# Optimization experiments

Measured on AMD Instinct MI355X. Metric: run time of the kernel, lower is better.

## Reference

```python
import jax, jax.numpy as jnp
import numpy as np

B, L, D, Y = 8, 2500, 512, 8921


def setup_inputs() -> dict:
    key = jax.random.key(0)
    k1, k2, k3, k4, k5, k6 = jax.random.split(key, 6)
    x = jax.random.normal(k1, (B, L, D), dtype=jnp.float32)
    target = jax.random.uniform(k2, (B, Y), dtype=jnp.float32)
    text_inputs = jax.random.randint(k3, (B, L), 0, 50000, dtype=jnp.int32)
    # Xavier-uniform-like init for the two [Y, D] weights
    lim = float(np.sqrt(6.0 / (Y + D)))
    U_weight = jax.random.uniform(k4, (Y, D), dtype=jnp.float32, minval=-lim, maxval=lim)
    final_weight = jax.random.uniform(k5, (Y, D), dtype=jnp.float32, minval=-lim, maxval=lim)
    final_bias = jax.random.uniform(k6, (Y,), dtype=jnp.float32, minval=-0.05, maxval=0.05)
    return {"x": x, "target": target, "text_inputs": text_inputs,
            "U_weight": U_weight, "final_weight": final_weight, "final_bias": final_bias}


def reference(x, target, text_inputs, U_weight, final_weight, final_bias):
    # att: [B, Y, L] = U.weight @ x^T
    att = jnp.einsum('yd,bld->byl', U_weight, x)
    # softmax over sequence dim
    alpha = jax.nn.softmax(att, axis=2)
    # per-label context: [B, Y, D]
    m = jnp.einsum('byl,bld->byd', alpha, x)
    # gated reduction instead of a linear layer: [B, Y]
    y = jnp.einsum('byd,yd->by', m, final_weight) + final_bias
    # BCEWithLogitsLoss (mean over all elements), numerically stable
    loss = jnp.mean(jnp.maximum(y, 0.0) - y * target + jnp.log1p(jnp.exp(-jnp.abs(y))))
    return (y, loss)
```

## Files before the change

kernel.cpp:

```cpp
#include <hip/hip_runtime.h>
#include <stdint.h>

#define B_ 8
#define L_ 2500
#define D_ 512
#define Y_ 8921
#define LP 2560
#define YP 8960
#define BLK 128
#define BK 32
#define NKT 16
#define NS 4
#define LTS 5
#define NBLK (70 * B_ * NS)
#define PERX (NBLK / 8)

typedef float f32x4 __attribute__((ext_vector_type(4)));
typedef __bf16 bf16x8 __attribute__((ext_vector_type(8)));
typedef unsigned short u16;
typedef unsigned int u32;

__device__ __forceinline__ u32 pack2(float a, float b) {
  u32 ua = __float_as_uint(a); ua = (ua + 0x7FFFu + ((ua >> 16) & 1u)) >> 16;
  u32 ub = __float_as_uint(b); ub = (ub + 0x7FFFu + ((ub >> 16) & 1u)) >> 16;
  return ua | (ub << 16);
}

__global__ void cvt_x_kernel(const float* __restrict__ x, u16* __restrict__ xb) {
  int idx = blockIdx.x * 256 + threadIdx.x;
  int row = idx >> 6;
  int c8  = (idx & 63) << 3;
  int b = row / LP;
  int l = row - b * LP;
  uint4 o;
  if (l < L_) {
    const float* s = x + (size_t)(b * L_ + l) * D_ + c8;
    float4 f0 = *(const float4*)s;
    float4 f1 = *(const float4*)(s + 4);
    o.x = pack2(f0.x, f0.y); o.y = pack2(f0.z, f0.w);
    o.z = pack2(f1.x, f1.y); o.w = pack2(f1.z, f1.w);
  } else {
    o = make_uint4(0u, 0u, 0u, 0u);
  }
  *(uint4*)(xb + (size_t)row * D_ + c8) = o;
}

__global__ void cvt_w_kernel(const float* __restrict__ U, const float* __restrict__ Wf,
                             u16* __restrict__ Ub, u16* __restrict__ Wb) {
  int idx = blockIdx.x * 256 + threadIdx.x;
  const int half = YP * 64;
  const float* src = U; u16* dst = Ub;
  int i = idx;
  if (idx >= half) { i -= half; src = Wf; dst = Wb; }
  int row = i >> 6;
  int c8  = (i & 63) << 3;
  uint4 o;
  if (row < Y_) {
    const float* s = src + (size_t)row * D_ + c8;
    float4 f0 = *(const float4*)s;
    float4 f1 = *(const float4*)(s + 4);
    o.x = pack2(f0.x, f0.y); o.y = pack2(f0.z, f0.w);
    o.z = pack2(f1.x, f1.y); o.w = pack2(f1.z, f1.w);
  } else {
    o = make_uint4(0u, 0u, 0u, 0u);
  }
  *(uint4*)(dst + (size_t)row * D_ + c8) = o;
}

__device__ __forceinline__ void async16(const u16* g, u16* l) {
  __builtin_amdgcn_global_load_lds(
      (const __attribute__((address_space(1))) u32*)g,
      (__attribute__((address_space(3))) u32*)l, 16, 0, 0);
}

__global__ __launch_bounds__(256, 2) void fused_kernel(
    const u16* __restrict__ xb,
    const u16* __restrict__ Ub,
    const u16* __restrict__ Wb,
    float* __restrict__ part)
{
  __shared__ __align__(16) u16 sX[BLK * BK];

  const int t    = threadIdx.x;
  const int lane = t & 63;
  const int wv   = t >> 6;
  const int l16  = lane & 15;
  const int q    = lane >> 4;

  const int bid = blockIdx.x;
  const int w   = (bid & 7) * PERX + (bid >> 3);
  const int yt  = w >> 5;
  const int rem = w & 31;
  const int b   = rem >> 2;
  const int s   = rem & 3;
  const int y0  = yt * BLK;

  const int srow = t >> 2;
  const int scol = (t & 3) << 3;
  const u16* gXb = xb + (size_t)b * LP * D_ + (size_t)srow * D_ + scol;
  u16* lX0 = sX + t * 8;
  u16* lX1 = sX + 2048 + t * 8;

  const u16* fU0 = Ub + (size_t)(y0 + wv * 32 + l16) * D_ + q * 8;
  const u16* fU1 = fU0 + (size_t)16 * D_;
  const u16* fW0 = Wb + (size_t)(y0 + wv * 32 + l16) * D_ + q * 8;
  const u16* fW1 = fW0 + (size_t)16 * D_;

  float M[8], Z[8], W[8];
#pragma unroll
  for (int i = 0; i < 8; ++i) { M[i] = -1e30f; Z[i] = 0.f; W[i] = 0.f; }

  const f32x4 z4 = {0.f, 0.f, 0.f, 0.f};

  for (int ltl = 0; ltl < LTS; ++ltl) {
    const int l0 = (s * LTS + ltl) * BLK;
    const u16* gX0 = gXb + (size_t)l0 * D_;
    const u16* gX1 = gX0 + (size_t)64 * D_;

    f32x4 accA[2][8], accS[2][8];
#pragma unroll
    for (int ry = 0; ry < 2; ++ry)
#pragma unroll
      for (int cl = 0; cl < 8; ++cl) { accA[ry][cl] = z4; accS[ry][cl] = z4; }

#pragma unroll 1
    for (int kt = 0; kt < NKT; ++kt) {
      const int ko = kt * BK;
      bf16x8 aU0 = *(const bf16x8*)(const void*)(fU0 + ko);
      bf16x8 aU1 = *(const bf16x8*)(const void*)(fU1 + ko);
      bf16x8 aW0 = *(const bf16x8*)(const void*)(fW0 + ko);
      bf16x8 aW1 = *(const bf16x8*)(const void*)(fW1 + ko);
      __syncthreads();
      async16(gX0 + ko, lX0);
      async16(gX1 + ko, lX1);
      __syncthreads();

#pragma unroll
      for (int cl = 0; cl < 8; ++cl) {
        bf16x8 bX = *(const bf16x8*)(const void*)(sX + (cl * 16 + l16) * BK + q * 8);
        accA[0][cl] = __builtin_amdgcn_mfma_f32_16x16x32_bf16(aU0, bX, accA[0][cl], 0, 0, 0);
        accA[1][cl] = __builtin_amdgcn_mfma_f32_16x16x32_bf16(aU1, bX, accA[1][cl], 0, 0, 0);
        accS[0][cl] = __builtin_amdgcn_mfma_f32_16x16x32_bf16(aW0, bX, accS[0][cl], 0, 0, 0);
        accS[1][cl] = __builtin_amdgcn_mfma_f32_16x16x32_bf16(aW1, bX, accS[1][cl], 0, 0, 0);
      }
    }

    const bool boundary = (l0 + BLK > L_);
#pragma unroll
    for (int ry = 0; ry < 2; ++ry) {
#pragma unroll
      for (int r = 0; r < 4; ++r) {
        const int si = ry * 4 + r;
        float a[8];
        if (boundary) {
#pragma unroll
          for (int cl = 0; cl < 8; ++cl) {
            float v = accA[ry][cl][r];
            a[cl] = (l0 + cl * 16 + l16 >= L_) ? -1e30f : v;
          }
        } else {
#pragma unroll
          for (int cl = 0; cl < 8; ++cl) a[cl] = accA[ry][cl][r];
        }
        float tmax = a[0];
#pragma unroll
        for (int cl = 1; cl < 8; ++cl) tmax = fmaxf(tmax, a[cl]);
        const float mnew  = fmaxf(M[si], tmax);
        const float scale = __expf(M[si] - mnew);
        float zl = 0.f, wl = 0.f;
#pragma unroll
        for (int cl = 0; cl < 8; ++cl) {
          float p = __expf(a[cl] - mnew);
          zl += p;
          wl = fmaf(p, accS[ry][cl][r], wl);
        }
        Z[si] = fmaf(Z[si], scale, zl);
        W[si] = fmaf(W[si], scale, wl);
        M[si] = mnew;
      }
    }
  }

#pragma unroll
  for (int si = 0; si < 8; ++si) {
    float M0 = M[si], Z0 = Z[si], W0 = W[si];
#pragma unroll
    for (int st = 1; st <= 8; st <<= 1) {
      const float Mo = __shfl_xor(M0, st);
      const float Zo = __shfl_xor(Z0, st);
      const float Wo = __shfl_xor(W0, st);
      const float mn = fmaxf(M0, Mo);
      const float sa = __expf(M0 - mn);
      const float sb = __expf(Mo - mn);
      Z0 = Z0 * sa + Zo * sb;
      W0 = W0 * sa + Wo * sb;
      M0 = mn;
    }
    M[si] = M0; Z[si] = Z0; W[si] = W0;
  }

  if (l16 == 0) {
    float* p = part + ((size_t)(b * 70 + yt) * NS + s) * 384;
#pragma unroll
    for (int ry = 0; ry < 2; ++ry) {
#pragma unroll
      for (int r = 0; r < 4; ++r) {
        const int si = ry * 4 + r;
        const int yl = wv * 32 + ry * 16 + q * 4 + r;
        p[yl]       = M[si];
        p[128 + yl] = Z[si];
        p[256 + yl] = W[si];
      }
    }
  }
}

__global__ void combine_kernel(const float* __restrict__ part,
                               const float* __restrict__ bias,
                               const float* __restrict__ target,
                               float* __restrict__ out) {
  const int idx = blockIdx.x * 256 + threadIdx.x;
  float lpart = 0.f;
  if (idx < B_ * Y_) {
    const int b = idx / Y_;
    const int y = idx - b * Y_;
    const int yt = y >> 7, yl = y & 127;
    const float* p = part + ((size_t)(b * 70 + yt) * NS) * 384 + yl;
    float M = -1e30f;
#pragma unroll
    for (int s2 = 0; s2 < NS; ++s2) M = fmaxf(M, p[s2 * 384]);
    float Z = 0.f, W = 0.f;
#pragma unroll
    for (int s2 = 0; s2 < NS; ++s2) {
      const float e = __expf(p[s2 * 384] - M);
      Z = fmaf(p[s2 * 384 + 128], e, Z);
      W = fmaf(p[s2 * 384 + 256], e, W);
    }
    const float yv = W / Z + bias[y];
    out[idx] = yv;
    const float tg = target[idx];
    lpart = fmaxf(yv, 0.f) - yv * tg + log1pf(__expf(-fabsf(yv)));
  }
  lpart += __shfl_xor(lpart, 1);  lpart += __shfl_xor(lpart, 2);
  lpart += __shfl_xor(lpart, 4);  lpart += __shfl_xor(lpart, 8);
  lpart += __shfl_xor(lpart, 16); lpart += __shfl_xor(lpart, 32);
  if ((threadIdx.x & 63) == 0)
    atomicAdd(out + (size_t)B_ * Y_, lpart * (1.0f / (B_ * Y_)));
}

extern "C" void kernel_launch(void* const* d_in, const int* in_sizes, int n_in,
                              void* d_out, int out_size, void* d_ws, size_t ws_size,
                              hipStream_t stream) {
  const float* x      = (const float*)d_in[0];
  const float* target = (const float*)d_in[1];
  const float* U      = (const float*)d_in[3];
  const float* Wf     = (const float*)d_in[4];
  const float* bias   = (const float*)d_in[5];
  float* out = (float*)d_out;

  u16* xb = (u16*)d_ws;
  u16* Ub = xb + (size_t)B_ * LP * D_;
  u16* Wb = Ub + (size_t)YP * D_;
  float* part = (float*)(Wb + (size_t)YP * D_);

  hipMemsetAsync(out + (size_t)B_ * Y_, 0, sizeof(float), stream);
  cvt_x_kernel<<<dim3((B_ * LP * 64) / 256), 256, 0, stream>>>(x, xb);
  cvt_w_kernel<<<dim3((2 * YP * 64) / 256), 256, 0, stream>>>(U, Wf, Ub, Wb);
  fused_kernel<<<dim3(NBLK), 256, 0, stream>>>(xb, Ub, Wb, part);
  combine_kernel<<<dim3((B_ * Y_ + 255) / 256), 256, 0, stream>>>(part, bias, target, out);
}
```

Baseline: 604.0 us.

## Add warp-specialized producer wave with 4-slot LDS ring for U, W and X tiles

Adds a fifth wave that streams the U, W and X bf16 tiles into a four-deep LDS ring buffer using async global-to-LDS loads. The four compute waves wait on per-slot ready counters instead of block-wide barriers and signal done counters. The A operands now come from LDS instead of per-thread global loads. The aim is to overlap memory transfer with MFMA work and drop the two __syncthreads per k-step. In exchange, occupancy drops to one 320-thread block per CU, the ring uses about 96KB of LDS, and the spin-wait flag protocol adds some correctness risk.

```diff
diff --git a/kernel.cpp b/kernel.cpp
--- a/kernel.cpp
+++ b/kernel.cpp
@@ -12,6 +12,9 @@
 #define NKT 16
 #define NS 4
 #define LTS 5
+#define NSLOT (LTS * NKT)
+#define RING 4
+#define SLOTU16 12288
 #define NBLK (70 * B_ * NS)
 #define PERX (NBLK / 8)
 
@@ -73,19 +76,19 @@
       (__attribute__((address_space(3))) u32*)l, 16, 0, 0);
 }
 
-__global__ __launch_bounds__(256, 2) void fused_kernel(
+__global__ __launch_bounds__(320, 1) void fused_kernel(
     const u16* __restrict__ xb,
     const u16* __restrict__ Ub,
     const u16* __restrict__ Wb,
     float* __restrict__ part)
 {
-  __shared__ __align__(16) u16 sX[BLK * BK];
+  __shared__ __align__(16) u16 sRing[RING * SLOTU16];
+  __shared__ unsigned ready[RING];
+  __shared__ unsigned done[RING];
 
   const int t    = threadIdx.x;
   const int lane = t & 63;
   const int wv   = t >> 6;
-  const int l16  = lane & 15;
-  const int q    = lane >> 4;
 
   const int bid = blockIdx.x;
   const int w   = (bid & 7) * PERX + (bid >> 3);
@@ -95,56 +98,104 @@
   const int s   = rem & 3;
   const int y0  = yt * BLK;
 
-  const int srow = t >> 2;
-  const int scol = (t & 3) << 3;
-  const u16* gXb = xb + (size_t)b * LP * D_ + (size_t)srow * D_ + scol;
-  u16* lX0 = sX + t * 8;
-  u16* lX1 = sX + 2048 + t * 8;
-
-  const u16* fU0 = Ub + (size_t)(y0 + wv * 32 + l16) * D_ + q * 8;
-  const u16* fU1 = fU0 + (size_t)16 * D_;
-  const u16* fW0 = Wb + (size_t)(y0 + wv * 32 + l16) * D_ + q * 8;
-  const u16* fW1 = fW0 + (size_t)16 * D_;
+  if (t < RING)            ready[t] = 0u;
+  else if (t < 2 * RING)   done[t - RING] = 0u;
+  __syncthreads();
+
+  if (wv == 4) {
+    const int p = lane;
+    const u16* bU = Ub + (size_t)(y0 + (p >> 2)) * D_ + (p & 3) * 8;
+    const u16* bW = Wb + (size_t)(y0 + (p >> 2)) * D_ + (p & 3) * 8;
+    const u16* bX = xb + ((size_t)b * LP + s * (LTS * BLK) + (p >> 2)) * D_ + (p & 3) * 8;
+    u16* lbase = sRing + p * 8;
+
+#pragma unroll 1
+    for (int n = 0; n < NSLOT; ++n) {
+      const int buf = n & (RING - 1);
+      const unsigned round = (unsigned)(n >> 2);
+      if (round > 0) {
+        while (((volatile unsigned*)done)[buf] < 4u * round)
+          __builtin_amdgcn_s_sleep(1);
+      }
+      asm volatile("" ::: "memory");
+      const int kt  = n & (NKT - 1);
+      const int ltl = n >> 4;
+      u16* dst = lbase + buf * SLOTU16;
+      const u16* pu = bU + kt * BK;
+      const u16* pw = bW + kt * BK;
+      const u16* px = bX + (size_t)(ltl * BLK) * D_ + kt * BK;
+#pragma unroll
+      for (int j8 = 0; j8 < 8; ++j8) {
+        async16(pu + (size_t)(j8 * 16) * D_, dst + j8 * 512);
+        async16(pw + (size_t)(j8 * 16) * D_, dst + 4096 + j8 * 512);
+        async16(px + (size_t)(j8 * 16) * D_, dst + 8192 + j8 * 512);
+      }
+      if (n >= 1) {
+        asm volatile("s_waitcnt vmcnt(24)" ::: "memory");
+        const int pb = (n - 1) & (RING - 1);
+        ((volatile unsigned*)ready)[pb] = (unsigned)(((n - 1) >> 2) + 1);
+        asm volatile("" ::: "memory");
+      }
+    }
+    asm volatile("s_waitcnt vmcnt(0)" ::: "memory");
+    ((volatile unsigned*)ready)[(NSLOT - 1) & (RING - 1)] =
+        (unsigned)(((NSLOT - 1) >> 2) + 1);
+    return;
+  }
+
+  const int l16 = lane & 15;
+  const int q   = lane >> 4;
+  const int offU = (wv * 32 + l16) * BK + q * 8;
 
   float M[8], Z[8], W[8];
 #pragma unroll
   for (int i = 0; i < 8; ++i) { M[i] = -1e30f; Z[i] = 0.f; W[i] = 0.f; }
 
   const f32x4 z4 = {0.f, 0.f, 0.f, 0.f};
+  int n = 0;
 
   for (int ltl = 0; ltl < LTS; ++ltl) {
+    f32x4 accA[2][8], accS[2][8];
+#pragma unroll
+    for (int ry = 0; ry < 2; ++ry)
+#pragma unroll
+      for (int cl = 0; cl < 8; ++cl) { accA[ry][cl] = z4; accS[ry][cl] = z4; }
+
+#pragma unroll 1
+    for (int kt = 0; kt < NKT; ++kt, ++n) {
+      const int buf = n & (RING - 1);
+      const unsigned want = (unsigned)((n >> 2) + 1);
+      while (((volatile unsigned*)ready)[buf] < want)
+        __builtin_amdgcn_s_sleep(1);
+      asm volatile("" ::: "memory");
+      __builtin_amdgcn_sched_barrier(0);
+
+      const u16* bb = sRing + buf * SLOTU16;
+      bf16x8 aU0 = *(const bf16x8*)(const void*)(bb + offU);
+      bf16x8 aU1 = *(const bf16x8*)(const void*)(bb + offU + 16 * BK);
+      bf16x8 aW0 = *(const bf16x8*)(const void*)(bb + 4096 + offU);
+      bf16x8 aW1 = *(const bf16x8*)(const void*)(bb + 4096 + offU + 16 * BK);
+      bf16x8 xf[8];
+#pragma unroll
+      for (int cl = 0; cl < 8; ++cl)
+        xf[cl] = *(const bf16x8*)(const void*)(bb + 8192 + (cl * 16 + l16) * BK + q * 8);
+
+      __builtin_amdgcn_s_setprio(1);
+#pragma unroll
+      for (int cl = 0; cl < 8; ++cl) {
+        accA[0][cl] = __builtin_amdgcn_mfma_f32_16x16x32_bf16(aU0, xf[cl], accA[0][cl], 0, 0, 0);
+        accA[1][cl] = __builtin_amdgcn_mfma_f32_16x16x32_bf16(aU1, xf[cl], accA[1][cl], 0, 0, 0);
+        accS[0][cl] = __builtin_amdgcn_mfma_f32_16x16x32_bf16(aW0, xf[cl], accS[0][cl], 0, 0, 0);
+        accS[1][cl] = __builtin_amdgcn_mfma_f32_16x16x32_bf16(aW1, xf[cl], accS[1][cl], 0, 0, 0);
+      }
+      __builtin_amdgcn_s_setprio(0);
+
+      asm volatile("s_waitcnt lgkmcnt(0)" ::: "memory");
+      __builtin_amdgcn_sched_barrier(0);
+      if (lane == 0) atomicAdd(&done[buf], 1u);
+    }
+
     const int l0 = (s * LTS + ltl) * BLK;
-    const u16* gX0 = gXb + (size_t)l0 * D_;
-    const u16* gX1 = gX0 + (size_t)64 * D_;
-
-    f32x4 accA[2][8], accS[2][8];
-#pragma unroll
-    for (int ry = 0; ry < 2; ++ry)
-#pragma unroll
-      for (int cl = 0; cl < 8; ++cl) { accA[ry][cl] = z4; accS[ry][cl] = z4; }
-
-#pragma unroll 1
-    for (int kt = 0; kt < NKT; ++kt) {
-      const int ko = kt * BK;
-      bf16x8 aU0 = *(const bf16x8*)(const void*)(fU0 + ko);
-      bf16x8 aU1 = *(const bf16x8*)(const void*)(fU1 + ko);
-      bf16x8 aW0 = *(const bf16x8*)(const void*)(fW0 + ko);
-      bf16x8 aW1 = *(const bf16x8*)(const void*)(fW1 + ko);
-      __syncthreads();
-      async16(gX0 + ko, lX0);
-      async16(gX1 + ko, lX1);
-      __syncthreads();
-
-#pragma unroll
-      for (int cl = 0; cl < 8; ++cl) {
-        bf16x8 bX = *(const bf16x8*)(const void*)(sX + (cl * 16 + l16) * BK + q * 8);
-        accA[0][cl] = __builtin_amdgcn_mfma_f32_16x16x32_bf16(aU0, bX, accA[0][cl], 0, 0, 0);
-        accA[1][cl] = __builtin_amdgcn_mfma_f32_16x16x32_bf16(aU1, bX, accA[1][cl], 0, 0, 0);
-        accS[0][cl] = __builtin_amdgcn_mfma_f32_16x16x32_bf16(aW0, bX, accS[0][cl], 0, 0, 0);
-        accS[1][cl] = __builtin_amdgcn_mfma_f32_16x16x32_bf16(aW1, bX, accS[1][cl], 0, 0, 0);
-      }
-    }
-
     const bool boundary = (l0 + BLK > L_);
 #pragma unroll
     for (int ry = 0; ry < 2; ++ry) {
@@ -266,6 +317,6 @@
   hipMemsetAsync(out + (size_t)B_ * Y_, 0, sizeof(float), stream);
   cvt_x_kernel<<<dim3((B_ * LP * 64) / 256), 256, 0, stream>>>(x, xb);
   cvt_w_kernel<<<dim3((2 * YP * 64) / 256), 256, 0, stream>>>(U, Wf, Ub, Wb);
-  fused_kernel<<<dim3(NBLK), 256, 0, stream>>>(xb, Ub, Wb, part);
+  fused_kernel<<<dim3(NBLK), 320, 0, stream>>>(xb, Ub, Wb, part);
   combine_kernel<<<dim3((B_ * Y_ + 255) / 256), 256, 0, stream>>>(part, bias, target, out);
 }
```

Result: slower. 709.3 us (+17.4%).
